# Performance work log

Measured on AMD Instinct MI355X. Metric: run time of the kernel, lower is better.

## Reference

```python
import jax, jax.numpy as jnp
import numpy as np
from jax import lax

H = 50  # hidden size fixed by the module


def setup_inputs() -> dict:
    key = jax.random.key(0)
    ks = jax.random.split(key, 7)
    B, T, I = 512, 1000, 64
    s = 0.1
    return {
        "x": jax.random.normal(ks[0], (B, T, I), dtype=jnp.float32),
        "W_ih": jax.random.normal(ks[1], (4 * H, I), dtype=jnp.float32) * s,
        "W_hh": jax.random.normal(ks[2], (4 * H, H), dtype=jnp.float32) * s,
        "b_ih": jax.random.normal(ks[3], (4 * H,), dtype=jnp.float32) * s,
        "b_hh": jax.random.normal(ks[4], (4 * H,), dtype=jnp.float32) * s,
        "W_out": jax.random.normal(ks[5], (2, H), dtype=jnp.float32) * s,
        "b_out": jax.random.normal(ks[6], (2,), dtype=jnp.float32) * s,
    }


def _lstm_last_h(x, W_ih, W_hh, b_ih, b_hh):
    # x: [B, T, I]. Precompute input contribution to all gates: [B, T, 4H]
    xg = jnp.einsum("bti,gi->btg", x, W_ih) + b_ih + b_hh
    B = x.shape[0]
    h0 = jnp.zeros((B, H), dtype=x.dtype)
    c0 = jnp.zeros((B, H), dtype=x.dtype)

    def step(carry, xt):
        h, c = carry
        gates = xt + h @ W_hh.T  # [B, 4H]
        i, f, g, o = jnp.split(gates, 4, axis=-1)  # torch gate order i,f,g,o
        i = jax.nn.sigmoid(i)
        f = jax.nn.sigmoid(f)
        g = jnp.tanh(g)
        o = jax.nn.sigmoid(o)
        c = f * c + i * g
        h = o * jnp.tanh(c)
        return (h, c), None

    (h_last, _), _ = lax.scan(step, (h0, c0), jnp.swapaxes(xg, 0, 1))
    return h_last  # [B, H]


def reference(x, W_ih, W_hh, b_ih, b_hh, W_out, b_out):
    h = _lstm_last_h(x, W_ih, W_hh, b_ih, b_hh)
    return h @ W_out.T + b_out  # [B, 2]
```

## Files before the change

kernel.cpp:

```cpp
#include <hip/hip_runtime.h>
#include <math.h>


#define HSZ 50
#define ISZ 64
#define TSZ 1000

typedef float f32x2 __attribute__((ext_vector_type(2)));

__device__ __forceinline__ float dpp_xor1(float v) {
    return __int_as_float(__builtin_amdgcn_update_dpp(
        0, __float_as_int(v), 0xB1, 0xF, 0xF, true));
}
__device__ __forceinline__ float dpp_xor2(float v) {
    return __int_as_float(__builtin_amdgcn_update_dpp(
        0, __float_as_int(v), 0x4E, 0xF, 0xF, true));
}
__device__ __forceinline__ float dpp_rev(float v) {
    return __int_as_float(__builtin_amdgcn_update_dpp(
        0, __float_as_int(v), 0x1B, 0xF, 0xF, true));
}

#define LSTM_STEP(t, OFF, XR, XG)                                              \
  {                                                                            \
    if (rtid < 200) {                                                          \
                                      \
      f32x2 accA; accA.x = XG; accA.y = 0.0f;                                  \
      f32x2 accB; accB.x = 0.0f; accB.y = 0.0f;                                \
      const float4* h4 = (const float4*)(&hbuf[row][(OFF) & 1][0]);            \
      _Pragma("unroll")                                                        \
      for (int j = 0; j < 12; ++j) {                                           \
        float4 v = h4[j];                                                      \
        f32x2 lo; lo.x = v.x; lo.y = v.y;                                      \
        f32x2 hi; hi.x = v.z; hi.y = v.w;                                      \
        accA += lo * whh[2 * j];                                               \
        accB += hi * whh[2 * j + 1];                                           \
      }                                                                        \
      { f32x2 tl = *(const f32x2*)(&hbuf[row][(OFF) & 1][48]);                 \
        accA += tl * whh[24]; }                                                \
      float acc = (accA.x + accB.x) + (accA.y + accB.y);                       \
      float e  = __expf(-(acc * gmul));                                        \
      float sg = __builtin_amdgcn_rcpf(1.0f + e);                              \
      float a  = __builtin_fmaf(sg, gma, gmb);            \
      float fg = dpp_xor1(a);                 \
      float gg = dpp_xor2(a);                 \
      float og = dpp_rev(a);                  \
      c_reg = __builtin_fmaf(fg, c_reg, a * gg);      \
      float ep = __expf(2.0f * c_reg);                                         \
      float rr = __builtin_amdgcn_rcpf(1.0f + ep);                             \
      float hv = __builtin_fmaf(-2.0f * og, rr, og);         \
      if ((rtid & 3) == 0) hbuf[row][((OFF) + 1) & 1][u] = hv;                 \
            \
      if ((t) + (OFF) + 2 < TSZ) {                                             \
        f32x2 pA; pA.x = bias; pA.y = 0.0f;                                    \
        f32x2 pB; pB.x = 0.0f; pB.y = 0.0f;                                    \
        const float4* x4 = (const float4*)(&xbuf[row][((OFF) + 2) & 3][0]);    \
        _Pragma("unroll")                                                      \
        for (int i = 0; i < 16; ++i) {                                         \
          float4 v = x4[i];                                                    \
          f32x2 lo; lo.x = v.x; lo.y = v.y;                                    \
          f32x2 hi; hi.x = v.z; hi.y = v.w;                                    \
          pA += lo * wih[2 * i];                                               \
          pB += hi * wih[2 * i + 1];                                           \
        }                                                                      \
        XG = (pA.x + pB.x) + (pA.y + pB.y);                                    \
      }                                                                        \
    } else if (rtid >= 224) {                                                  \
      if ((t) + (OFF) + 3 < TSZ)                                               \
        *(f32x2*)(&xbuf[row][((OFF) + 3) & 3][2 * ll]) = XR;                   \
      if ((t) + (OFF) + 5 < TSZ)                                               \
        XR = *(const f32x2*)(xrow + (size_t)((t) + (OFF) + 5) * ISZ + 2 * ll); \
    }                                                                          \
                     \
    asm volatile("s_waitcnt lgkmcnt(0)" ::: "memory");                         \
    __builtin_amdgcn_s_barrier();                                              \
    __builtin_amdgcn_sched_barrier(0);                                         \
  }

__global__ __launch_bounds__(512, 2) void lstm_fused(
    const float* __restrict__ x,
    const float* __restrict__ W_ih,
    const float* __restrict__ W_hh,
    const float* __restrict__ b_ih,
    const float* __restrict__ b_hh,
    const float* __restrict__ W_out,
    const float* __restrict__ b_out,
    float* __restrict__ out)
{
    const int bb   = blockIdx.x;
    const int tid  = threadIdx.x;
    const int row  = tid >> 8;
    const int rtid = tid & 255;

    __shared__ __align__(16) float xbuf[2][4][ISZ];
    __shared__ __align__(16) float hbuf[2][2][56];

    const int g = rtid & 3;
    const int u = rtid >> 2;
    const int k = g * HSZ + u;
    const float gmul = (g == 2) ? 2.0f : 1.0f;
    const float gma  = (g == 2) ? 2.0f : 1.0f;
    const float gmb  = (g == 2) ? -1.0f : 0.0f;

    const int ll = rtid - 224;

    const float* xrow = x + (size_t)(2 * bb + row) * (TSZ * ISZ);

    f32x2 whh[25];
    f32x2 wih[32];
    float bias  = 0.0f;
    float c_reg = 0.0f;
    float xgA = 0.0f, xgB = 0.0f;
    f32x2 xr0; xr0.x = 0.0f; xr0.y = 0.0f;
    f32x2 xr1; xr1.x = 0.0f; xr1.y = 0.0f;

    if (rtid < 200) {
        const float* wh = W_hh + k * HSZ;
        #pragma unroll
        for (int j = 0; j < 25; ++j) whh[j] = *(const f32x2*)(wh + 2 * j);
        const float* wi = W_ih + k * ISZ;
        #pragma unroll
        for (int i = 0; i < 32; ++i) wih[i] = *(const f32x2*)(wi + 2 * i);
        bias = b_ih[k] + b_hh[k];
    } else if (ll >= 0) {
        #pragma unroll
        for (int n = 0; n < 3; ++n) {
            f32x2 v = *(const f32x2*)(xrow + n * ISZ + 2 * ll);
            *(f32x2*)(&xbuf[row][n][2 * ll]) = v;
        }
        xr0 = *(const f32x2*)(xrow + 3 * ISZ + 2 * ll);
        xr1 = *(const f32x2*)(xrow + 4 * ISZ + 2 * ll);
    }
    if (rtid < 56) { hbuf[row][0][rtid] = 0.0f; hbuf[row][1][rtid] = 0.0f; }
    __syncthreads();

    if (rtid < 200) {
        #pragma unroll
        for (int n = 0; n < 2; ++n) {
            f32x2 pA; pA.x = bias; pA.y = 0.0f;
            f32x2 pB; pB.x = 0.0f; pB.y = 0.0f;
            const float4* x4 = (const float4*)(&xbuf[row][n][0]);
            #pragma unroll
            for (int i = 0; i < 16; ++i) {
                float4 v = x4[i];
                f32x2 lo; lo.x = v.x; lo.y = v.y;
                f32x2 hi; hi.x = v.z; hi.y = v.w;
                pA += lo * wih[2 * i];
                pB += hi * wih[2 * i + 1];
            }
            float r = (pA.x + pB.x) + (pA.y + pB.y);
            if (n == 0) xgA = r; else xgB = r;
        }
    }

    for (int t = 0; t < TSZ; t += 4) {
        LSTM_STEP(t, 0, xr0, xgA)
        LSTM_STEP(t, 1, xr1, xgB)
        LSTM_STEP(t, 2, xr0, xgA)
        LSTM_STEP(t, 3, xr1, xgB)
    }

    if (rtid < 2) {
        float acc = b_out[rtid];
        const float* wo = W_out + rtid * HSZ;
        #pragma unroll
        for (int j = 0; j < HSZ; ++j) acc += hbuf[row][0][j] * wo[j];
        out[(2 * bb + row) * 2 + rtid] = acc;
    }
}

extern "C" void kernel_launch(void* const* d_in, const int* in_sizes, int n_in,
                              void* d_out, int out_size, void* d_ws, size_t ws_size,
                              hipStream_t stream) {
    const float* x     = (const float*)d_in[0];
    const float* W_ih  = (const float*)d_in[1];
    const float* W_hh  = (const float*)d_in[2];
    const float* b_ih  = (const float*)d_in[3];
    const float* b_hh  = (const float*)d_in[4];
    const float* W_out = (const float*)d_in[5];
    const float* b_out = (const float*)d_in[6];
    float* out = (float*)d_out;

    const int B = in_sizes[0] / (TSZ * ISZ);
    hipLaunchKernelGGL(lstm_fused, dim3(B / 2), dim3(512), 0, stream,
                       x, W_ih, W_hh, b_ih, b_hh, W_out, b_out, out);
}
```

Baseline: 771.2 us.

## Process both batch rows per thread in a 256-thread block, sharing weight registers

Each workgroup shrinks from 512 to 256 threads, and every gate thread now advances two batch rows per time step using the same W_hh/W_ih registers. The goal is to halve the number of threads holding weights and to make each per-step barrier cover twice the work. The global x prefetch distance grows from 5 to 7 steps, using four rotating register pairs per row. In exchange, the serial dependency chain per step is roughly twice as long inside each wave, and occupancy per CU changes.

```diff
diff --git a/kernel.cpp b/kernel.cpp
--- a/kernel.cpp
+++ b/kernel.cpp
@@ -21,55 +21,63 @@
         0, __float_as_int(v), 0x1B, 0xF, 0xF, true));
 }
 
-#define LSTM_STEP(t, OFF, XR, XG)                                              \
+#define ROW_STEP(R, C, XG, OFF, t)                                             \
   {                                                                            \
-    if (rtid < 200) {                                                          \
-                                      \
-      f32x2 accA; accA.x = XG; accA.y = 0.0f;                                  \
-      f32x2 accB; accB.x = 0.0f; accB.y = 0.0f;                                \
-      const float4* h4 = (const float4*)(&hbuf[row][(OFF) & 1][0]);            \
+    f32x2 accA; accA.x = XG; accA.y = 0.0f;                                    \
+    f32x2 accB; accB.x = 0.0f; accB.y = 0.0f;                                  \
+    const float4* h4 = (const float4*)(&hbuf[R][(OFF) & 1][0]);                \
+    _Pragma("unroll")                                                          \
+    for (int j = 0; j < 12; ++j) {                                             \
+      float4 v = h4[j];                                                        \
+      f32x2 lo; lo.x = v.x; lo.y = v.y;                                        \
+      f32x2 hi; hi.x = v.z; hi.y = v.w;                                        \
+      accA += lo * whh[2 * j];                                                 \
+      accB += hi * whh[2 * j + 1];                                             \
+    }                                                                          \
+    { f32x2 tl = *(const f32x2*)(&hbuf[R][(OFF) & 1][48]);                     \
+      accA += tl * whh[24]; }                                                  \
+    float acc = (accA.x + accB.x) + (accA.y + accB.y);                         \
+    float e  = __expf(-(acc * gmul));                                          \
+    float sg = __builtin_amdgcn_rcpf(1.0f + e);                                \
+    float a  = __builtin_fmaf(sg, gma, gmb);              \
+    float fg = dpp_xor1(a);                                                    \
+    float gg = dpp_xor2(a);                                                    \
+    float og = dpp_rev(a);                                                     \
+    C = __builtin_fmaf(fg, C, a * gg);                \
+    float ep = __expf(2.0f * C);                                               \
+    float rr = __builtin_amdgcn_rcpf(1.0f + ep);                               \
+    float hv = __builtin_fmaf(-2.0f * og, rr, og);           \
+    if ((tid & 3) == 0) hbuf[R][((OFF) + 1) & 1][u] = hv;                      \
+    if ((t) + (OFF) + 2 < TSZ) {                                               \
+      f32x2 pA; pA.x = bias; pA.y = 0.0f;                                      \
+      f32x2 pB; pB.x = 0.0f; pB.y = 0.0f;                                      \
+      const float4* x4 = (const float4*)(&xbuf[R][((OFF) + 2) & 3][0]);        \
       _Pragma("unroll")                                                        \
-      for (int j = 0; j < 12; ++j) {                                           \
-        float4 v = h4[j];                                                      \
+      for (int i = 0; i < 16; ++i) {                                           \
+        float4 v = x4[i];                                                      \
         f32x2 lo; lo.x = v.x; lo.y = v.y;                                      \
         f32x2 hi; hi.x = v.z; hi.y = v.w;                                      \
-        accA += lo * whh[2 * j];                                               \
-        accB += hi * whh[2 * j + 1];                                           \
+        pA += lo * wih[2 * i];                                                 \
+        pB += hi * wih[2 * i + 1];                                             \
       }                                                                        \
-      { f32x2 tl = *(const f32x2*)(&hbuf[row][(OFF) & 1][48]);                 \
-        accA += tl * whh[24]; }                                                \
-      float acc = (accA.x + accB.x) + (accA.y + accB.y);                       \
-      float e  = __expf(-(acc * gmul));                                        \
-      float sg = __builtin_amdgcn_rcpf(1.0f + e);                              \
-      float a  = __builtin_fmaf(sg, gma, gmb);            \
-      float fg = dpp_xor1(a);                 \
-      float gg = dpp_xor2(a);                 \
-      float og = dpp_rev(a);                  \
-      c_reg = __builtin_fmaf(fg, c_reg, a * gg);      \
-      float ep = __expf(2.0f * c_reg);                                         \
-      float rr = __builtin_amdgcn_rcpf(1.0f + ep);                             \
-      float hv = __builtin_fmaf(-2.0f * og, rr, og);         \
-      if ((rtid & 3) == 0) hbuf[row][((OFF) + 1) & 1][u] = hv;                 \
-            \
-      if ((t) + (OFF) + 2 < TSZ) {                                             \
-        f32x2 pA; pA.x = bias; pA.y = 0.0f;                                    \
-        f32x2 pB; pB.x = 0.0f; pB.y = 0.0f;                                    \
-        const float4* x4 = (const float4*)(&xbuf[row][((OFF) + 2) & 3][0]);    \
-        _Pragma("unroll")                                                      \
-        for (int i = 0; i < 16; ++i) {                                         \
-          float4 v = x4[i];                                                    \
-          f32x2 lo; lo.x = v.x; lo.y = v.y;                                    \
-          f32x2 hi; hi.x = v.z; hi.y = v.w;                                    \
-          pA += lo * wih[2 * i];                                               \
-          pB += hi * wih[2 * i + 1];                                           \
-        }                                                                      \
-        XG = (pA.x + pB.x) + (pA.y + pB.y);                                    \
+      XG = (pA.x + pB.x) + (pA.y + pB.y);                                      \
+    }                                                                          \
+  }
+
+#define LSTM_STEP(t, OFF, XR0, XR1, XG0, XG1)                                  \
+  {                                                                            \
+    if (tid < 200) {                                                           \
+      ROW_STEP(0, c0, XG0, OFF, t)                                             \
+      ROW_STEP(1, c1, XG1, OFF, t)                                             \
+    } else if (tid >= 224) {                                                   \
+      if ((t) + (OFF) + 3 < TSZ) {                                             \
+        *(f32x2*)(&xbuf[0][((OFF) + 3) & 3][2 * ll]) = XR0;                    \
+        *(f32x2*)(&xbuf[1][((OFF) + 3) & 3][2 * ll]) = XR1;                    \
       }                                                                        \
-    } else if (rtid >= 224) {                                                  \
-      if ((t) + (OFF) + 3 < TSZ)                                               \
-        *(f32x2*)(&xbuf[row][((OFF) + 3) & 3][2 * ll]) = XR;                   \
-      if ((t) + (OFF) + 5 < TSZ)                                               \
-        XR = *(const f32x2*)(xrow + (size_t)((t) + (OFF) + 5) * ISZ + 2 * ll); \
+      if ((t) + (OFF) + 7 < TSZ) {                                             \
+        XR0 = *(const f32x2*)(xrow0 + (size_t)((t) + (OFF) + 7) * ISZ + 2*ll); \
+        XR1 = *(const f32x2*)(xrow1 + (size_t)((t) + (OFF) + 7) * ISZ + 2*ll); \
+      }                                                                        \
     }                                                                          \
                      \
     asm volatile("s_waitcnt lgkmcnt(0)" ::: "memory");                         \
@@ -77,7 +85,7 @@
     __builtin_amdgcn_sched_barrier(0);                                         \
   }
 
-__global__ __launch_bounds__(512, 2) void lstm_fused(
+__global__ __launch_bounds__(256, 1) void lstm_fused(
     const float* __restrict__ x,
     const float* __restrict__ W_ih,
     const float* __restrict__ W_hh,
@@ -87,34 +95,34 @@
     const float* __restrict__ b_out,
     float* __restrict__ out)
 {
-    const int bb   = blockIdx.x;
-    const int tid  = threadIdx.x;
-    const int row  = tid >> 8;
-    const int rtid = tid & 255;
+    const int bb  = blockIdx.x;
+    const int tid = threadIdx.x;
 
     __shared__ __align__(16) float xbuf[2][4][ISZ];
     __shared__ __align__(16) float hbuf[2][2][56];
 
-    const int g = rtid & 3;
-    const int u = rtid >> 2;
+    const int g = tid & 3;
+    const int u = tid >> 2;
     const int k = g * HSZ + u;
     const float gmul = (g == 2) ? 2.0f : 1.0f;
     const float gma  = (g == 2) ? 2.0f : 1.0f;
     const float gmb  = (g == 2) ? -1.0f : 0.0f;
 
-    const int ll = rtid - 224;
-
-    const float* xrow = x + (size_t)(2 * bb + row) * (TSZ * ISZ);
+    const int ll = tid - 224;
+
+    const float* xrow0 = x + (size_t)(2 * bb)     * (TSZ * ISZ);
+    const float* xrow1 = x + (size_t)(2 * bb + 1) * (TSZ * ISZ);
 
     f32x2 whh[25];
     f32x2 wih[32];
-    float bias  = 0.0f;
-    float c_reg = 0.0f;
-    float xgA = 0.0f, xgB = 0.0f;
-    f32x2 xr0; xr0.x = 0.0f; xr0.y = 0.0f;
-    f32x2 xr1; xr1.x = 0.0f; xr1.y = 0.0f;
-
-    if (rtid < 200) {
+    float bias = 0.0f;
+    float c0 = 0.0f, c1 = 0.0f;
+    float xgE0 = 0.0f, xgE1 = 0.0f;
+    float xgO0 = 0.0f, xgO1 = 0.0f;
+    f32x2 xrA0{}, xrA1{}, xrA2{}, xrA3{};
+    f32x2 xrB0{}, xrB1{}, xrB2{}, xrB3{};
+
+    if (tid < 200) {
         const float* wh = W_hh + k * HSZ;
         #pragma unroll
         for (int j = 0; j < 25; ++j) whh[j] = *(const f32x2*)(wh + 2 * j);
@@ -125,47 +133,63 @@
     } else if (ll >= 0) {
         #pragma unroll
         for (int n = 0; n < 3; ++n) {
-            f32x2 v = *(const f32x2*)(xrow + n * ISZ + 2 * ll);
-            *(f32x2*)(&xbuf[row][n][2 * ll]) = v;
+            *(f32x2*)(&xbuf[0][n][2 * ll]) =
+                *(const f32x2*)(xrow0 + (size_t)n * ISZ + 2 * ll);
+            *(f32x2*)(&xbuf[1][n][2 * ll]) =
+                *(const f32x2*)(xrow1 + (size_t)n * ISZ + 2 * ll);
         }
-        xr0 = *(const f32x2*)(xrow + 3 * ISZ + 2 * ll);
-        xr1 = *(const f32x2*)(xrow + 4 * ISZ + 2 * ll);
-    }
-    if (rtid < 56) { hbuf[row][0][rtid] = 0.0f; hbuf[row][1][rtid] = 0.0f; }
+        xrA0 = *(const f32x2*)(xrow0 + 3 * (size_t)ISZ + 2 * ll);
+        xrA1 = *(const f32x2*)(xrow0 + 4 * (size_t)ISZ + 2 * ll);
+        xrA2 = *(const f32x2*)(xrow0 + 5 * (size_t)ISZ + 2 * ll);
+        xrA3 = *(const f32x2*)(xrow0 + 6 * (size_t)ISZ + 2 * ll);
+        xrB0 = *(const f32x2*)(xrow1 + 3 * (size_t)ISZ + 2 * ll);
+        xrB1 = *(const f32x2*)(xrow1 + 4 * (size_t)ISZ + 2 * ll);
+        xrB2 = *(const f32x2*)(xrow1 + 5 * (size_t)ISZ + 2 * ll);
+        xrB3 = *(const f32x2*)(xrow1 + 6 * (size_t)ISZ + 2 * ll);
+    }
+    if (tid < 56) {
+        hbuf[0][0][tid] = 0.0f; hbuf[0][1][tid] = 0.0f;
+        hbuf[1][0][tid] = 0.0f; hbuf[1][1][tid] = 0.0f;
+    }
     __syncthreads();
 
-    if (rtid < 200) {
-        #pragma unroll
-        for (int n = 0; n < 2; ++n) {
-            f32x2 pA; pA.x = bias; pA.y = 0.0f;
-            f32x2 pB; pB.x = 0.0f; pB.y = 0.0f;
-            const float4* x4 = (const float4*)(&xbuf[row][n][0]);
+    if (tid < 200) {
+        #pragma unroll
+        for (int R = 0; R < 2; ++R) {
             #pragma unroll
-            for (int i = 0; i < 16; ++i) {
-                float4 v = x4[i];
-                f32x2 lo; lo.x = v.x; lo.y = v.y;
-                f32x2 hi; hi.x = v.z; hi.y = v.w;
-                pA += lo * wih[2 * i];
-                pB += hi * wih[2 * i + 1];
+            for (int n = 0; n < 2; ++n) {
+                f32x2 pA; pA.x = bias; pA.y = 0.0f;
+                f32x2 pB; pB.x = 0.0f; pB.y = 0.0f;
+                const float4* x4 = (const float4*)(&xbuf[R][n][0]);
+                #pragma unroll
+                for (int i = 0; i < 16; ++i) {
+                    float4 v = x4[i];
+                    f32x2 lo; lo.x = v.x; lo.y = v.y;
+                    f32x2 hi; hi.x = v.z; hi.y = v.w;
+                    pA += lo * wih[2 * i];
+                    pB += hi * wih[2 * i + 1];
+                }
+                float r = (pA.x + pB.x) + (pA.y + pB.y);
+                if (R == 0) { if (n == 0) xgE0 = r; else xgO0 = r; }
+                else        { if (n == 0) xgE1 = r; else xgO1 = r; }
             }
-            float r = (pA.x + pB.x) + (pA.y + pB.y);
-            if (n == 0) xgA = r; else xgB = r;
         }
     }
 
     for (int t = 0; t < TSZ; t += 4) {
-        LSTM_STEP(t, 0, xr0, xgA)
-        LSTM_STEP(t, 1, xr1, xgB)
-        LSTM_STEP(t, 2, xr0, xgA)
-        LSTM_STEP(t, 3, xr1, xgB)
-    }
-
-    if (rtid < 2) {
-        float acc = b_out[rtid];
-        const float* wo = W_out + rtid * HSZ;
-        #pragma unroll
-        for (int j = 0; j < HSZ; ++j) acc += hbuf[row][0][j] * wo[j];
-        out[(2 * bb + row) * 2 + rtid] = acc;
+        LSTM_STEP(t, 0, xrA0, xrB0, xgE0, xgE1)
+        LSTM_STEP(t, 1, xrA1, xrB1, xgO0, xgO1)
+        LSTM_STEP(t, 2, xrA2, xrB2, xgE0, xgE1)
+        LSTM_STEP(t, 3, xrA3, xrB3, xgO0, xgO1)
+    }
+
+    if (tid < 4) {
+        const int R = tid >> 1, o = tid & 1;
+        float acc = b_out[o];
+        const float* wo = W_out + o * HSZ;
+        #pragma unroll
+        for (int j = 0; j < HSZ; ++j) acc += hbuf[R][0][j] * wo[j];
+        out[(2 * bb + R) * 2 + o] = acc;
     }
 }
 
@@ -182,6 +206,6 @@
     float* out = (float*)d_out;
 
     const int B = in_sizes[0] / (TSZ * ISZ);
-    hipLaunchKernelGGL(lstm_fused, dim3(B / 2), dim3(512), 0, stream,
+    hipLaunchKernelGGL(lstm_fused, dim3(B / 2), dim3(256), 0, stream,
                        x, W_ih, W_hh, b_ih, b_hh, W_out, b_out, out);
 }
```

Measured after the change: 1.140 ms. 47.8% more time.

## Run one batch row per 256-thread block and deepen x prefetch to four steps

Applied to the files above, without the earlier changes.

The kernel now launches one block of 256 threads per batch row instead of packing two rows into a 512-thread block, so the per-step barrier only synchronises the waves of a single row. The global x prefetch for the loader threads is extended from two to four register slots, so loads are issued seven steps ahead instead of five to hide more memory latency. This doubles the number of blocks. Each block still reserves roughly the same per-thread register budget, so residency per CU depends on how the new launch bounds map to occupancy.

```diff
diff --git a/kernel.cpp b/kernel.cpp
--- a/kernel.cpp
+++ b/kernel.cpp
@@ -23,11 +23,11 @@
 
 #define LSTM_STEP(t, OFF, XR, XG)                                              \
   {                                                                            \
-    if (rtid < 200) {                                                          \
+    if (tid < 200) {                                                           \
                                       \
       f32x2 accA; accA.x = XG; accA.y = 0.0f;                                  \
       f32x2 accB; accB.x = 0.0f; accB.y = 0.0f;                                \
-      const float4* h4 = (const float4*)(&hbuf[row][(OFF) & 1][0]);            \
+      const float4* h4 = (const float4*)(&hbuf[(OFF) & 1][0]);                 \
       _Pragma("unroll")                                                        \
       for (int j = 0; j < 12; ++j) {                                           \
         float4 v = h4[j];                                                      \
@@ -36,25 +36,25 @@
         accA += lo * whh[2 * j];                                               \
         accB += hi * whh[2 * j + 1];                                           \
       }                                                                        \
-      { f32x2 tl = *(const f32x2*)(&hbuf[row][(OFF) & 1][48]);                 \
+      { f32x2 tl = *(const f32x2*)(&hbuf[(OFF) & 1][48]);                      \
         accA += tl * whh[24]; }                                                \
       float acc = (accA.x + accB.x) + (accA.y + accB.y);                       \
       float e  = __expf(-(acc * gmul));                                        \
       float sg = __builtin_amdgcn_rcpf(1.0f + e);                              \
       float a  = __builtin_fmaf(sg, gma, gmb);            \
-      float fg = dpp_xor1(a);                 \
-      float gg = dpp_xor2(a);                 \
-      float og = dpp_rev(a);                  \
+      float fg = dpp_xor1(a);                                                  \
+      float gg = dpp_xor2(a);                                                  \
+      float og = dpp_rev(a);                                                   \
       c_reg = __builtin_fmaf(fg, c_reg, a * gg);      \
       float ep = __expf(2.0f * c_reg);                                         \
       float rr = __builtin_amdgcn_rcpf(1.0f + ep);                             \
       float hv = __builtin_fmaf(-2.0f * og, rr, og);         \
-      if ((rtid & 3) == 0) hbuf[row][((OFF) + 1) & 1][u] = hv;                 \
+      if ((tid & 3) == 0) hbuf[((OFF) + 1) & 1][u] = hv;                       \
             \
       if ((t) + (OFF) + 2 < TSZ) {                                             \
         f32x2 pA; pA.x = bias; pA.y = 0.0f;                                    \
         f32x2 pB; pB.x = 0.0f; pB.y = 0.0f;                                    \
-        const float4* x4 = (const float4*)(&xbuf[row][((OFF) + 2) & 3][0]);    \
+        const float4* x4 = (const float4*)(&xbuf[((OFF) + 2) & 3][0]);         \
         _Pragma("unroll")                                                      \
         for (int i = 0; i < 16; ++i) {                                         \
           float4 v = x4[i];                                                    \
@@ -65,11 +65,11 @@
         }                                                                      \
         XG = (pA.x + pB.x) + (pA.y + pB.y);                                    \
       }                                                                        \
-    } else if (rtid >= 224) {                                                  \
+    } else if (tid >= 224) {                                                   \
       if ((t) + (OFF) + 3 < TSZ)                                               \
-        *(f32x2*)(&xbuf[row][((OFF) + 3) & 3][2 * ll]) = XR;                   \
-      if ((t) + (OFF) + 5 < TSZ)                                               \
-        XR = *(const f32x2*)(xrow + (size_t)((t) + (OFF) + 5) * ISZ + 2 * ll); \
+        *(f32x2*)(&xbuf[((OFF) + 3) & 3][2 * ll]) = XR;                        \
+      if ((t) + (OFF) + 7 < TSZ)                                               \
+        XR = *(const f32x2*)(xrow + (size_t)((t) + (OFF) + 7) * ISZ + 2 * ll); \
     }                                                                          \
                      \
     asm volatile("s_waitcnt lgkmcnt(0)" ::: "memory");                         \
@@ -77,7 +77,7 @@
     __builtin_amdgcn_sched_barrier(0);                                         \
   }
 
-__global__ __launch_bounds__(512, 2) void lstm_fused(
+__global__ __launch_bounds__(256, 2) void lstm_fused(
     const float* __restrict__ x,
     const float* __restrict__ W_ih,
     const float* __restrict__ W_hh,
@@ -87,34 +87,31 @@
     const float* __restrict__ b_out,
     float* __restrict__ out)
 {
-    const int bb   = blockIdx.x;
-    const int tid  = threadIdx.x;
-    const int row  = tid >> 8;
-    const int rtid = tid & 255;
+    const int row = blockIdx.x;
+    const int tid = threadIdx.x;
 
-    __shared__ __align__(16) float xbuf[2][4][ISZ];
-    __shared__ __align__(16) float hbuf[2][2][56];
+    __shared__ __align__(16) float xbuf[4][ISZ];
+    __shared__ __align__(16) float hbuf[2][56];
 
-    const int g = rtid & 3;
-    const int u = rtid >> 2;
+    const int g = tid & 3;
+    const int u = tid >> 2;
     const int k = g * HSZ + u;
     const float gmul = (g == 2) ? 2.0f : 1.0f;
     const float gma  = (g == 2) ? 2.0f : 1.0f;
     const float gmb  = (g == 2) ? -1.0f : 0.0f;
 
-    const int ll = rtid - 224;
+    const int ll = tid - 224;
 
-    const float* xrow = x + (size_t)(2 * bb + row) * (TSZ * ISZ);
+    const float* xrow = x + (size_t)row * (TSZ * ISZ);
 
     f32x2 whh[25];
     f32x2 wih[32];
     float bias  = 0.0f;
     float c_reg = 0.0f;
-    float xgA = 0.0f, xgB = 0.0f;
-    f32x2 xr0; xr0.x = 0.0f; xr0.y = 0.0f;
-    f32x2 xr1; xr1.x = 0.0f; xr1.y = 0.0f;
+    float xgE = 0.0f, xgO = 0.0f;
+    f32x2 xr0{}, xr1{}, xr2{}, xr3{};
 
-    if (rtid < 200) {
+    if (tid < 200) {
         const float* wh = W_hh + k * HSZ;
         #pragma unroll
         for (int j = 0; j < 25; ++j) whh[j] = *(const f32x2*)(wh + 2 * j);
@@ -125,21 +122,23 @@
     } else if (ll >= 0) {
         #pragma unroll
         for (int n = 0; n < 3; ++n) {
-            f32x2 v = *(const f32x2*)(xrow + n * ISZ + 2 * ll);
-            *(f32x2*)(&xbuf[row][n][2 * ll]) = v;
+            *(f32x2*)(&xbuf[n][2 * ll]) =
+                *(const f32x2*)(xrow + (size_t)n * ISZ + 2 * ll);
         }
-        xr0 = *(const f32x2*)(xrow + 3 * ISZ + 2 * ll);
-        xr1 = *(const f32x2*)(xrow + 4 * ISZ + 2 * ll);
+        xr0 = *(const f32x2*)(xrow + 3 * (size_t)ISZ + 2 * ll);
+        xr1 = *(const f32x2*)(xrow + 4 * (size_t)ISZ + 2 * ll);
+        xr2 = *(const f32x2*)(xrow + 5 * (size_t)ISZ + 2 * ll);
+        xr3 = *(const f32x2*)(xrow + 6 * (size_t)ISZ + 2 * ll);
     }
-    if (rtid < 56) { hbuf[row][0][rtid] = 0.0f; hbuf[row][1][rtid] = 0.0f; }
+    if (tid < 56) { hbuf[0][tid] = 0.0f; hbuf[1][tid] = 0.0f; }
     __syncthreads();
 
-    if (rtid < 200) {
+    if (tid < 200) {
         #pragma unroll
         for (int n = 0; n < 2; ++n) {
             f32x2 pA; pA.x = bias; pA.y = 0.0f;
             f32x2 pB; pB.x = 0.0f; pB.y = 0.0f;
-            const float4* x4 = (const float4*)(&xbuf[row][n][0]);
+            const float4* x4 = (const float4*)(&xbuf[n][0]);
             #pragma unroll
             for (int i = 0; i < 16; ++i) {
                 float4 v = x4[i];
@@ -149,23 +148,23 @@
                 pB += hi * wih[2 * i + 1];
             }
             float r = (pA.x + pB.x) + (pA.y + pB.y);
-            if (n == 0) xgA = r; else xgB = r;
+            if (n == 0) xgE = r; else xgO = r;
         }
     }
 
     for (int t = 0; t < TSZ; t += 4) {
-        LSTM_STEP(t, 0, xr0, xgA)
-        LSTM_STEP(t, 1, xr1, xgB)
-        LSTM_STEP(t, 2, xr0, xgA)
-        LSTM_STEP(t, 3, xr1, xgB)
+        LSTM_STEP(t, 0, xr0, xgE)
+        LSTM_STEP(t, 1, xr1, xgO)
+        LSTM_STEP(t, 2, xr2, xgE)
+        LSTM_STEP(t, 3, xr3, xgO)
     }
 
-    if (rtid < 2) {
-        float acc = b_out[rtid];
-        const float* wo = W_out + rtid * HSZ;
+    if (tid < 2) {
+        float acc = b_out[tid];
+        const float* wo = W_out + tid * HSZ;
         #pragma unroll
-        for (int j = 0; j < HSZ; ++j) acc += hbuf[row][0][j] * wo[j];
-        out[(2 * bb + row) * 2 + rtid] = acc;
+        for (int j = 0; j < HSZ; ++j) acc += hbuf[0][j] * wo[j];
+        out[row * 2 + tid] = acc;
     }
 }
 
@@ -182,6 +181,6 @@
     float* out = (float*)d_out;
 
     const int B = in_sizes[0] / (TSZ * ISZ);
-    hipLaunchKernelGGL(lstm_fused, dim3(B / 2), dim3(512), 0, stream,
+    hipLaunchKernelGGL(lstm_fused, dim3(B), dim3(256), 0, stream,
                        x, W_ih, W_hh, b_ih, b_hh, W_out, b_out, out);
 }
```

New measurement: 759.4 us. No clear change (-1.5%).
